# Kernel optimization log

Measured on AMD Instinct MI355X. Metric: run time of the kernel, lower is better.

The kernel has to match this reference:

```python
import jax, jax.numpy as jnp
import numpy as np

TEMP = 0.07
EPS = 1e-8
NUM_CLASSES = 7
THRESH = 0.3


def setup_inputs() -> dict:
    key = jax.random.key(0)
    k1, k2, k3, k4, k5 = jax.random.split(key, 5)
    N, H, E, C = 8192, 128, 256, NUM_CLASSES
    reps = jax.random.normal(k1, (N, H), dtype=jnp.float32)
    labels = jax.random.randint(k2, (N,), 0, C, dtype=jnp.int64 if jax.config.jax_enable_x64 else jnp.int32)
    centers = jax.random.normal(k3, (C, E), dtype=jnp.float32)
    fc_w = jax.random.normal(k4, (H, E), dtype=jnp.float32) * (1.0 / np.sqrt(E))
    fc_b = jax.random.normal(k5, (H,), dtype=jnp.float32) * 0.01
    return {"reps": reps, "labels": labels, "centers": centers, "fc_w": fc_w, "fc_b": fc_b}


def reference(reps, labels, centers, fc_w, fc_b):
    # fc(default_centers): [C, H]
    curr_centers = centers @ fc_w.T + fc_b
    pad_labels = jnp.arange(NUM_CLASSES, dtype=labels.dtype)

    all_reps = jnp.concatenate([reps, curr_centers], axis=0)      # [M, H]
    all_labels = jnp.concatenate([labels, pad_labels], axis=0)    # [M]
    B = reps.shape[0]
    M = all_reps.shape[0]

    # cosine similarity via normalized matmul (avoids [B,M,H] broadcast)
    norms = jnp.sqrt(jnp.sum(all_reps * all_reps, axis=-1))
    rn = all_reps / jnp.maximum(norms, 1e-8)[:, None]
    cos = rn[:B] @ rn.T                                           # [B, M]

    scores = (1.0 + cos) * 0.5 + EPS
    eye = (jnp.arange(B)[:, None] == jnp.arange(M)[None, :]).astype(scores.dtype)
    scores = scores * (1.0 - eye) / TEMP
    # torch uses .item() on the max -> a non-differentiable constant
    scores = scores - jax.lax.stop_gradient(jnp.max(scores))
    e = jnp.exp(scores)

    pos_mask = (labels[:, None] == all_labels[None, :]).astype(scores.dtype)  # [B, M]
    mask = 1.0 - eye

    pos_sum = jnp.sum(e * pos_mask * mask, axis=-1)
    neg_sum = jnp.sum(e * (1.0 - pos_mask), axis=-1)
    probs = pos_sum / (pos_sum + neg_sum)
    probs = probs / (jnp.sum(pos_mask * mask, axis=-1) + EPS)

    loss_vec = -jnp.log(probs + EPS)
    loss_mask = (loss_vec > THRESH).astype(loss_vec.dtype)
    denom = jax.lax.stop_gradient(jnp.sum(loss_mask)) + EPS
    loss = jnp.sum(loss_vec * loss_mask) / denom
    return loss
```

## Files before the change

kernel.cpp:

```cpp
#include <hip/hip_runtime.h>
#include <hip/hip_bf16.h>

#define BN 8192
#define MM 8199
#define MP 8208
#define HH 128
#define EE 256
#define NTILE 513
#define JCHUNKS 64
#define NUM_HIST 7

typedef __attribute__((ext_vector_type(8))) short short8;
typedef __attribute__((ext_vector_type(4))) float floatx4;

__global__ __launch_bounds__(256)
void centers_kernel(const float* __restrict__ centers,
                    const float* __restrict__ fc_w,
                    const float* __restrict__ fc_b,
                    float* __restrict__ curr) {
  int wid = threadIdx.x >> 6, lane = threadIdx.x & 63;
  int o = (blockIdx.x << 2) | wid;
  int c = o >> 7, h = o & 127;
  const float4* ce = (const float4*)(centers + c * EE);
  const float4* w  = (const float4*)(fc_w + h * EE);
  float4 a = ce[lane];
  float4 b = w[lane];
  float s = a.x * b.x + a.y * b.y + a.z * b.z + a.w * b.w;
#pragma unroll
  for (int m = 1; m < 64; m <<= 1) s += __shfl_xor(s, m);
  if (lane == 0) curr[o] = s + fc_b[h];
}

__global__ __launch_bounds__(256)
void norm_kernel(const float* __restrict__ reps,
                 const float* __restrict__ curr,
                 const int* __restrict__ labels,
                 __hip_bfloat16* __restrict__ rn,
                 int* __restrict__ labp) {
  int wid = threadIdx.x >> 6, lane = threadIdx.x & 63;
  int r = (blockIdx.x << 2) | wid;
  float2 v = make_float2(0.f, 0.f);
  if (r < BN)      v = ((const float2*)(reps + (size_t)r * HH))[lane];
  else if (r < MM) v = ((const float2*)(curr + (size_t)(r - BN) * HH))[lane];
  float ss = v.x * v.x + v.y * v.y;
#pragma unroll
  for (int m = 1; m < 64; m <<= 1) ss += __shfl_xor(ss, m);
  float inv = 1.0f / fmaxf(sqrtf(ss), 1e-8f);
  __hip_bfloat162 h2;
  h2.x = __float2bfloat16(v.x * inv);
  h2.y = __float2bfloat16(v.y * inv);
  ((__hip_bfloat162*)(rn + (size_t)r * HH))[lane] = h2;
  if (lane == 0) labp[r] = (r < BN) ? labels[r] : (r < MM ? r - BN : -1);
}

__global__ __launch_bounds__(256, 2)
void main_kernel(const __hip_bfloat16* __restrict__ rn,
                 const int* __restrict__ labp,
                 float* __restrict__ tot,
                 float* __restrict__ pos) {
  __shared__ float red[128];
  const int lane = threadIdx.x & 63;
  const int wid  = threadIdx.x >> 6;
  const int q = lane >> 4, col = lane & 15;
  const int ibase = blockIdx.x * 64;
  const int chunk = (blockIdx.y << 2) | wid;
  const short* rns = (const short*)rn;

  if (threadIdx.x < 128) red[threadIdx.x] = 0.f;

  short8 afrag[4][4];
#pragma unroll
  for (int it = 0; it < 4; ++it) {
    const short8* p = (const short8*)(rns + (size_t)(ibase + it * 16 + col) * HH + q * 8);
    afrag[it][0] = p[0];
    afrag[it][1] = p[4];
    afrag[it][2] = p[8];
    afrag[it][3] = p[12];
  }
  int labi[4][4];
#pragma unroll
  for (int it = 0; it < 4; ++it)
#pragma unroll
    for (int r = 0; r < 4; ++r)
      labi[it][r] = labp[ibase + it * 16 + q * 4 + r];

  float stot[4][4] = {};
  float spos[4][4] = {};
  const float K2 = 10.30496147f;

  const short* bptr = rns + (chunk * 16 + col) * HH + q * 8;
  const int* lptr = labp + chunk * 16 + col;

  for (int jb = chunk * 16; jb < MP; jb += 16 * JCHUNKS) {
    short8 b0 = ((const short8*)bptr)[0];
    short8 b1 = ((const short8*)bptr)[4];
    short8 b2 = ((const short8*)bptr)[8];
    short8 b3 = ((const short8*)bptr)[12];
    const int labj = *lptr;
    bptr += 16 * JCHUNKS * HH;
    lptr += 16 * JCHUNKS;
#pragma unroll
    for (int it = 0; it < 4; ++it) {
      floatx4 acc = {0.f, 0.f, 0.f, 0.f};
      acc = __builtin_amdgcn_mfma_f32_16x16x32_bf16(afrag[it][0], b0, acc, 0, 0, 0);
      acc = __builtin_amdgcn_mfma_f32_16x16x32_bf16(afrag[it][1], b1, acc, 0, 0, 0);
      acc = __builtin_amdgcn_mfma_f32_16x16x32_bf16(afrag[it][2], b2, acc, 0, 0, 0);
      acc = __builtin_amdgcn_mfma_f32_16x16x32_bf16(afrag[it][3], b3, acc, 0, 0, 0);
      const bool isdiag = (jb == ibase + it * 16);
#pragma unroll
      for (int r = 0; r < 4; ++r) {
        float e = exp2f(fmaf(acc[r], K2, -K2));
        if (isdiag && (col == q * 4 + r)) e = 0.f;
        stot[it][r] += e;
        spos[it][r] += (labj == labi[it][r]) ? e : 0.f;
      }
    }
  }

  __syncthreads();

#pragma unroll
  for (int it = 0; it < 4; ++it)
#pragma unroll
    for (int r = 0; r < 4; ++r) {
      float tt = stot[it][r], pp = spos[it][r];
#pragma unroll
      for (int m = 1; m <= 8; m <<= 1) {
        tt += __shfl_xor(tt, m);
        pp += __shfl_xor(pp, m);
      }
      if (col == 0) {
        int li = it * 16 + q * 4 + r;
        atomicAdd(&red[li], tt);
        atomicAdd(&red[64 + li], pp);
      }
    }
  __syncthreads();
  if (threadIdx.x < 64)       atomicAdd(&tot[ibase + threadIdx.x], red[threadIdx.x]);
  else if (threadIdx.x < 128) atomicAdd(&pos[ibase + threadIdx.x - 64], red[threadIdx.x]);
}

__global__ __launch_bounds__(1024)
void loss_kernel(const float* __restrict__ tot,
                 const float* __restrict__ pos,
                 const int* __restrict__ labels,
                 float* __restrict__ out) {
  __shared__ int hist[NUM_HIST];
  __shared__ float s1[16], s2[16];
  const int tid = threadIdx.x;
  const int lane = tid & 63, wid = tid >> 6;
  if (tid < NUM_HIST) hist[tid] = 0;
  __syncthreads();
  int cnt0 = 0, cnt1 = 0, cnt2 = 0, cnt3 = 0, cnt4 = 0, cnt5 = 0, cnt6 = 0;
  for (int i = tid; i < BN; i += 1024) {
    int lab = labels[i];
    unsigned long long m0 = __ballot(lab == 0);
    unsigned long long m1 = __ballot(lab == 1);
    unsigned long long m2 = __ballot(lab == 2);
    unsigned long long m3 = __ballot(lab == 3);
    unsigned long long m4 = __ballot(lab == 4);
    unsigned long long m5 = __ballot(lab == 5);
    unsigned long long m6 = __ballot(lab == 6);
    if (lane == 0) {
      cnt0 += __popcll(m0); cnt1 += __popcll(m1); cnt2 += __popcll(m2);
      cnt3 += __popcll(m3); cnt4 += __popcll(m4); cnt5 += __popcll(m5);
      cnt6 += __popcll(m6);
    }
  }
  if (lane == 0) {
    atomicAdd(&hist[0], cnt0); atomicAdd(&hist[1], cnt1);
    atomicAdd(&hist[2], cnt2); atomicAdd(&hist[3], cnt3);
    atomicAdd(&hist[4], cnt4); atomicAdd(&hist[5], cnt5);
    atomicAdd(&hist[6], cnt6);
  }
  __syncthreads();
  const float K2 = 10.30496147f;
  const float epad = exp2f(-K2);
  float lsum = 0.f, msum = 0.f;
  for (int i = tid; i < BN; i += 1024) {
    float t = tot[i] - 9.0f * epad;
    float p = pos[i];
    float c = (float)hist[labels[i]];
    float pr = (p / t) / (c + 1e-8f);
    float lv = -logf(pr + 1e-8f);
    if (lv > 0.3f) { lsum += lv; msum += 1.f; }
  }
#pragma unroll
  for (int m = 1; m < 64; m <<= 1) {
    lsum += __shfl_xor(lsum, m);
    msum += __shfl_xor(msum, m);
  }
  if (lane == 0) { s1[wid] = lsum; s2[wid] = msum; }
  __syncthreads();
  if (wid == 0) {
    float a = (lane < 16) ? s1[lane] : 0.f;
    float b = (lane < 16) ? s2[lane] : 0.f;
#pragma unroll
    for (int m = 1; m < 16; m <<= 1) {
      a += __shfl_xor(a, m);
      b += __shfl_xor(b, m);
    }
    if (lane == 0) out[0] = a / (b + 1e-8f);
  }
}

extern "C" void kernel_launch(void* const* d_in, const int* in_sizes, int n_in,
                              void* d_out, int out_size, void* d_ws, size_t ws_size,
                              hipStream_t stream) {
  const float* reps    = (const float*)d_in[0];
  const int*   labels  = (const int*)d_in[1];
  const float* centers = (const float*)d_in[2];
  const float* fc_w    = (const float*)d_in[3];
  const float* fc_b    = (const float*)d_in[4];
  float* out = (float*)d_out;

  char* ws = (char*)d_ws;
  float* curr = (float*)ws;
  int* labp   = (int*)(ws + 4096);
  __hip_bfloat16* rn = (__hip_bfloat16*)(ws + 40960);
  float* tot = (float*)(ws + 40960 + 2101248);
  float* pos = tot + BN;

  hipMemsetAsync(tot, 0, 2 * BN * sizeof(float), stream);
  centers_kernel<<<224, 256, 0, stream>>>(centers, fc_w, fc_b, curr);
  norm_kernel<<<2052, 256, 0, stream>>>(reps, curr, labels, rn, labp);
  main_kernel<<<dim3(128, 16), 256, 0, stream>>>(rn, labp, tot, pos);
  loss_kernel<<<1, 1024, 0, stream>>>(tot, pos, labels, out);
}
```

Baseline: 138.2 us.

## Fuse prep kernels and loss into main kernel, prefetch B fragments

Merges the centers projection and normalization into one prep kernel that also zeroes the accumulators, replacing the memset. The final loss reduction moves into the main kernel via a last-block-done atomic counter, which drops one launch. The main loop software-prefetches the next B fragment and uses the raw hardware exp2 intrinsic. These cut launch overhead and hide load latency, at the cost of relying on correct fence/atomic ordering in the last block.

```diff
diff --git a/kernel.cpp b/kernel.cpp
--- a/kernel.cpp
+++ b/kernel.cpp
@@ -6,59 +6,84 @@
 #define MP 8208
 #define HH 128
 #define EE 256
-#define NTILE 513
 #define JCHUNKS 64
+#define GX 128
+#define GY 16
+#define NBLK (GX * GY)
 #define NUM_HIST 7
 
 typedef __attribute__((ext_vector_type(8))) short short8;
 typedef __attribute__((ext_vector_type(4))) float floatx4;
 
 __global__ __launch_bounds__(256)
-void centers_kernel(const float* __restrict__ centers,
-                    const float* __restrict__ fc_w,
-                    const float* __restrict__ fc_b,
-                    float* __restrict__ curr) {
-  int wid = threadIdx.x >> 6, lane = threadIdx.x & 63;
-  int o = (blockIdx.x << 2) | wid;
-  int c = o >> 7, h = o & 127;
-  const float4* ce = (const float4*)(centers + c * EE);
-  const float4* w  = (const float4*)(fc_w + h * EE);
-  float4 a = ce[lane];
-  float4 b = w[lane];
-  float s = a.x * b.x + a.y * b.y + a.z * b.z + a.w * b.w;
-#pragma unroll
-  for (int m = 1; m < 64; m <<= 1) s += __shfl_xor(s, m);
-  if (lane == 0) curr[o] = s + fc_b[h];
-}
-
-__global__ __launch_bounds__(256)
-void norm_kernel(const float* __restrict__ reps,
-                 const float* __restrict__ curr,
+void prep_kernel(const float* __restrict__ reps,
                  const int* __restrict__ labels,
+                 const float* __restrict__ centers,
+                 const float* __restrict__ fc_w,
+                 const float* __restrict__ fc_b,
                  __hip_bfloat16* __restrict__ rn,
-                 int* __restrict__ labp) {
-  int wid = threadIdx.x >> 6, lane = threadIdx.x & 63;
-  int r = (blockIdx.x << 2) | wid;
-  float2 v = make_float2(0.f, 0.f);
-  if (r < BN)      v = ((const float2*)(reps + (size_t)r * HH))[lane];
-  else if (r < MM) v = ((const float2*)(curr + (size_t)(r - BN) * HH))[lane];
-  float ss = v.x * v.x + v.y * v.y;
-#pragma unroll
-  for (int m = 1; m < 64; m <<= 1) ss += __shfl_xor(ss, m);
-  float inv = 1.0f / fmaxf(sqrtf(ss), 1e-8f);
-  __hip_bfloat162 h2;
-  h2.x = __float2bfloat16(v.x * inv);
-  h2.y = __float2bfloat16(v.y * inv);
-  ((__hip_bfloat162*)(rn + (size_t)r * HH))[lane] = h2;
-  if (lane == 0) labp[r] = (r < BN) ? labels[r] : (r < MM ? r - BN : -1);
+                 int* __restrict__ labp,
+                 float* __restrict__ tot,
+                 int* __restrict__ bcount) {
+  const int wid = threadIdx.x >> 6, lane = threadIdx.x & 63;
+  const int b = blockIdx.x;
+  if (b < 2048) {
+    if (threadIdx.x < 8) tot[b * 8 + threadIdx.x] = 0.f;
+    const int r = b * 4 + wid;
+    float2 v = ((const float2*)(reps + (size_t)r * HH))[lane];
+    float ss = v.x * v.x + v.y * v.y;
+#pragma unroll
+    for (int m = 1; m < 64; m <<= 1) ss += __shfl_xor(ss, m);
+    float inv = 1.0f / fmaxf(sqrtf(ss), 1e-8f);
+    __hip_bfloat162 h2;
+    h2.x = __float2bfloat16(v.x * inv);
+    h2.y = __float2bfloat16(v.y * inv);
+    ((__hip_bfloat162*)(rn + (size_t)r * HH))[lane] = h2;
+    if (lane == 0) labp[r] = labels[r];
+  } else {
+    __shared__ float currs[7 * HH];
+    if (threadIdx.x == 0) *bcount = 0;
+    for (int o = threadIdx.x; o < 7 * HH; o += 256) {
+      int c = o >> 7, h = o & 127;
+      const float4* ce = (const float4*)(centers + c * EE);
+      const float4* w  = (const float4*)(fc_w + h * EE);
+      float s = 0.f;
+#pragma unroll 4
+      for (int j = 0; j < EE / 4; ++j) {
+        float4 a = ce[j], bb = w[j];
+        s += a.x * bb.x + a.y * bb.y + a.z * bb.z + a.w * bb.w;
+      }
+      currs[o] = s + fc_b[h];
+    }
+    __syncthreads();
+    for (int k = 0; k < 4; ++k) {
+      int c = wid * 4 + k;
+      int r = BN + c;
+      float2 v = make_float2(0.f, 0.f);
+      if (c < 7) v = ((const float2*)(currs + c * HH))[lane];
+      float ss = v.x * v.x + v.y * v.y;
+#pragma unroll
+      for (int m = 1; m < 64; m <<= 1) ss += __shfl_xor(ss, m);
+      float inv = 1.0f / fmaxf(sqrtf(ss), 1e-8f);
+      __hip_bfloat162 h2;
+      h2.x = __float2bfloat16(v.x * inv);
+      h2.y = __float2bfloat16(v.y * inv);
+      ((__hip_bfloat162*)(rn + (size_t)r * HH))[lane] = h2;
+      if (lane == 0) labp[r] = (r < MM) ? r - BN : -1;
+    }
+  }
 }
 
 __global__ __launch_bounds__(256, 2)
 void main_kernel(const __hip_bfloat16* __restrict__ rn,
                  const int* __restrict__ labp,
+                 const int* __restrict__ labels,
                  float* __restrict__ tot,
-                 float* __restrict__ pos) {
+                 float* __restrict__ pos,
+                 int* __restrict__ bcount,
+                 float* __restrict__ out) {
   __shared__ float red[128];
+  __shared__ int amlast;
   const int lane = threadIdx.x & 63;
   const int wid  = threadIdx.x >> 6;
   const int q = lane >> 4, col = lane & 15;
@@ -88,33 +113,45 @@
   float spos[4][4] = {};
   const float K2 = 10.30496147f;
 
-  const short* bptr = rns + (chunk * 16 + col) * HH + q * 8;
-  const int* lptr = labp + chunk * 16 + col;
-
-  for (int jb = chunk * 16; jb < MP; jb += 16 * JCHUNKS) {
-    short8 b0 = ((const short8*)bptr)[0];
-    short8 b1 = ((const short8*)bptr)[4];
-    short8 b2 = ((const short8*)bptr)[8];
-    short8 b3 = ((const short8*)bptr)[12];
-    const int labj = *lptr;
-    bptr += 16 * JCHUNKS * HH;
-    lptr += 16 * JCHUNKS;
+  const short* bptr = rns + (size_t)(chunk * 16 + col) * HH + q * 8;
+  short8 bc0 = ((const short8*)bptr)[0];
+  short8 bc1 = ((const short8*)bptr)[4];
+  short8 bc2 = ((const short8*)bptr)[8];
+  short8 bc3 = ((const short8*)bptr)[12];
+  int labj = labp[chunk * 16 + col];
+  int jb = chunk * 16;
+
+  while (true) {
+    const int jn = jb + 16 * JCHUNKS;
+    const bool more = (jn < MP);
+    const short* np = more ? (bptr + 16 * JCHUNKS * HH) : (rns + col * HH + q * 8);
+    short8 n0 = ((const short8*)np)[0];
+    short8 n1 = ((const short8*)np)[4];
+    short8 n2 = ((const short8*)np)[8];
+    short8 n3 = ((const short8*)np)[12];
+    const int labn = labp[more ? jn + col : col];
+
 #pragma unroll
     for (int it = 0; it < 4; ++it) {
       floatx4 acc = {0.f, 0.f, 0.f, 0.f};
-      acc = __builtin_amdgcn_mfma_f32_16x16x32_bf16(afrag[it][0], b0, acc, 0, 0, 0);
-      acc = __builtin_amdgcn_mfma_f32_16x16x32_bf16(afrag[it][1], b1, acc, 0, 0, 0);
-      acc = __builtin_amdgcn_mfma_f32_16x16x32_bf16(afrag[it][2], b2, acc, 0, 0, 0);
-      acc = __builtin_amdgcn_mfma_f32_16x16x32_bf16(afrag[it][3], b3, acc, 0, 0, 0);
+      acc = __builtin_amdgcn_mfma_f32_16x16x32_bf16(afrag[it][0], bc0, acc, 0, 0, 0);
+      acc = __builtin_amdgcn_mfma_f32_16x16x32_bf16(afrag[it][1], bc1, acc, 0, 0, 0);
+      acc = __builtin_amdgcn_mfma_f32_16x16x32_bf16(afrag[it][2], bc2, acc, 0, 0, 0);
+      acc = __builtin_amdgcn_mfma_f32_16x16x32_bf16(afrag[it][3], bc3, acc, 0, 0, 0);
       const bool isdiag = (jb == ibase + it * 16);
 #pragma unroll
       for (int r = 0; r < 4; ++r) {
-        float e = exp2f(fmaf(acc[r], K2, -K2));
+        float e = __builtin_amdgcn_exp2f(fmaf(acc[r], K2, -K2));
         if (isdiag && (col == q * 4 + r)) e = 0.f;
         stot[it][r] += e;
         spos[it][r] += (labj == labi[it][r]) ? e : 0.f;
       }
     }
+    if (!more) break;
+    jb = jn;
+    bptr = np;
+    bc0 = n0; bc1 = n1; bc2 = n2; bc3 = n3;
+    labj = labn;
   }
 
   __syncthreads();
@@ -138,21 +175,24 @@
   __syncthreads();
   if (threadIdx.x < 64)       atomicAdd(&tot[ibase + threadIdx.x], red[threadIdx.x]);
   else if (threadIdx.x < 128) atomicAdd(&pos[ibase + threadIdx.x - 64], red[threadIdx.x]);
-}
-
-__global__ __launch_bounds__(1024)
-void loss_kernel(const float* __restrict__ tot,
-                 const float* __restrict__ pos,
-                 const int* __restrict__ labels,
-                 float* __restrict__ out) {
+
+  __threadfence();
+  __syncthreads();
+  if (threadIdx.x == 0) {
+    int old = atomicAdd(bcount, 1);
+    amlast = (old == NBLK - 1) ? 1 : 0;
+  }
+  __syncthreads();
+  if (!amlast) return;
+  __threadfence();
+
   __shared__ int hist[NUM_HIST];
-  __shared__ float s1[16], s2[16];
+  __shared__ float s1[4], s2[4];
   const int tid = threadIdx.x;
-  const int lane = tid & 63, wid = tid >> 6;
   if (tid < NUM_HIST) hist[tid] = 0;
   __syncthreads();
-  int cnt0 = 0, cnt1 = 0, cnt2 = 0, cnt3 = 0, cnt4 = 0, cnt5 = 0, cnt6 = 0;
-  for (int i = tid; i < BN; i += 1024) {
+  int c0 = 0, c1 = 0, c2 = 0, c3 = 0, c4 = 0, c5 = 0, c6 = 0;
+  for (int i = tid; i < BN; i += 256) {
     int lab = labels[i];
     unsigned long long m0 = __ballot(lab == 0);
     unsigned long long m1 = __ballot(lab == 1);
@@ -162,24 +202,22 @@
     unsigned long long m5 = __ballot(lab == 5);
     unsigned long long m6 = __ballot(lab == 6);
     if (lane == 0) {
-      cnt0 += __popcll(m0); cnt1 += __popcll(m1); cnt2 += __popcll(m2);
-      cnt3 += __popcll(m3); cnt4 += __popcll(m4); cnt5 += __popcll(m5);
-      cnt6 += __popcll(m6);
+      c0 += __popcll(m0); c1 += __popcll(m1); c2 += __popcll(m2);
+      c3 += __popcll(m3); c4 += __popcll(m4); c5 += __popcll(m5);
+      c6 += __popcll(m6);
     }
   }
   if (lane == 0) {
-    atomicAdd(&hist[0], cnt0); atomicAdd(&hist[1], cnt1);
-    atomicAdd(&hist[2], cnt2); atomicAdd(&hist[3], cnt3);
-    atomicAdd(&hist[4], cnt4); atomicAdd(&hist[5], cnt5);
-    atomicAdd(&hist[6], cnt6);
-  }
-  __syncthreads();
-  const float K2 = 10.30496147f;
-  const float epad = exp2f(-K2);
+    atomicAdd(&hist[0], c0); atomicAdd(&hist[1], c1); atomicAdd(&hist[2], c2);
+    atomicAdd(&hist[3], c3); atomicAdd(&hist[4], c4); atomicAdd(&hist[5], c5);
+    atomicAdd(&hist[6], c6);
+  }
+  __syncthreads();
+  const float epad9 = 9.0f * __builtin_amdgcn_exp2f(-K2);
   float lsum = 0.f, msum = 0.f;
-  for (int i = tid; i < BN; i += 1024) {
-    float t = tot[i] - 9.0f * epad;
-    float p = pos[i];
+  for (int i = tid; i < BN; i += 256) {
+    float t = __hip_atomic_load(&tot[i], __ATOMIC_RELAXED, __HIP_MEMORY_SCOPE_AGENT) - epad9;
+    float p = __hip_atomic_load(&pos[i], __ATOMIC_RELAXED, __HIP_MEMORY_SCOPE_AGENT);
     float c = (float)hist[labels[i]];
     float pr = (p / t) / (c + 1e-8f);
     float lv = -logf(pr + 1e-8f);
@@ -192,15 +230,10 @@
   }
   if (lane == 0) { s1[wid] = lsum; s2[wid] = msum; }
   __syncthreads();
-  if (wid == 0) {
-    float a = (lane < 16) ? s1[lane] : 0.f;
-    float b = (lane < 16) ? s2[lane] : 0.f;
-#pragma unroll
-    for (int m = 1; m < 16; m <<= 1) {
-      a += __shfl_xor(a, m);
-      b += __shfl_xor(b, m);
-    }
-    if (lane == 0) out[0] = a / (b + 1e-8f);
+  if (tid == 0) {
+    float a = s1[0] + s1[1] + s1[2] + s1[3];
+    float b = s2[0] + s2[1] + s2[2] + s2[3];
+    out[0] = a / (b + 1e-8f);
   }
 }
 
@@ -215,15 +248,13 @@
   float* out = (float*)d_out;
 
   char* ws = (char*)d_ws;
-  float* curr = (float*)ws;
+  int* bcount = (int*)(ws + 3584);
   int* labp   = (int*)(ws + 4096);
   __hip_bfloat16* rn = (__hip_bfloat16*)(ws + 40960);
   float* tot = (float*)(ws + 40960 + 2101248);
   float* pos = tot + BN;
 
-  hipMemsetAsync(tot, 0, 2 * BN * sizeof(float), stream);
-  centers_kernel<<<224, 256, 0, stream>>>(centers, fc_w, fc_b, curr);
-  norm_kernel<<<2052, 256, 0, stream>>>(reps, curr, labels, rn, labp);
-  main_kernel<<<dim3(128, 16), 256, 0, stream>>>(rn, labp, tot, pos);
-  loss_kernel<<<1, 1024, 0, stream>>>(tot, pos, labels, out);
+  prep_kernel<<<2049, 256, 0, stream>>>(reps, labels, centers, fc_w, fc_b,
+                                        rn, labp, tot, bcount);
+  main_kernel<<<dim3(GX, GY), 256, 0, stream>>>(rn, labp, labels, tot, pos, bcount, out);
 }
```

Measured after the change: 280.9 us. 2.03x slower.

## Fuse memset, center projection and normalization into one prep kernel; halve main tile rows

Applied to the files above, without the earlier changes.

Merges the memset, the centers projection kernel and the norm kernel into a single prep kernel. The last block computes the 7 projected centers in shared memory and normalizes them, which removes two launches and a memset. The main kernel now handles 32 rows per block instead of 64, doubling the grid to 256x16 for more parallelism. The price is more redundant B-fragment loads across blocks and a serial single-block centers computation.

```diff
diff --git a/kernel.cpp b/kernel.cpp
--- a/kernel.cpp
+++ b/kernel.cpp
@@ -6,51 +6,69 @@
 #define MP 8208
 #define HH 128
 #define EE 256
-#define NTILE 513
 #define JCHUNKS 64
+#define GX 256
+#define GY 16
 #define NUM_HIST 7
 
 typedef __attribute__((ext_vector_type(8))) short short8;
 typedef __attribute__((ext_vector_type(4))) float floatx4;
 
 __global__ __launch_bounds__(256)
-void centers_kernel(const float* __restrict__ centers,
-                    const float* __restrict__ fc_w,
-                    const float* __restrict__ fc_b,
-                    float* __restrict__ curr) {
-  int wid = threadIdx.x >> 6, lane = threadIdx.x & 63;
-  int o = (blockIdx.x << 2) | wid;
-  int c = o >> 7, h = o & 127;
-  const float4* ce = (const float4*)(centers + c * EE);
-  const float4* w  = (const float4*)(fc_w + h * EE);
-  float4 a = ce[lane];
-  float4 b = w[lane];
-  float s = a.x * b.x + a.y * b.y + a.z * b.z + a.w * b.w;
-#pragma unroll
-  for (int m = 1; m < 64; m <<= 1) s += __shfl_xor(s, m);
-  if (lane == 0) curr[o] = s + fc_b[h];
-}
-
-__global__ __launch_bounds__(256)
-void norm_kernel(const float* __restrict__ reps,
-                 const float* __restrict__ curr,
+void prep_kernel(const float* __restrict__ reps,
                  const int* __restrict__ labels,
+                 const float* __restrict__ centers,
+                 const float* __restrict__ fc_w,
+                 const float* __restrict__ fc_b,
                  __hip_bfloat16* __restrict__ rn,
-                 int* __restrict__ labp) {
-  int wid = threadIdx.x >> 6, lane = threadIdx.x & 63;
-  int r = (blockIdx.x << 2) | wid;
-  float2 v = make_float2(0.f, 0.f);
-  if (r < BN)      v = ((const float2*)(reps + (size_t)r * HH))[lane];
-  else if (r < MM) v = ((const float2*)(curr + (size_t)(r - BN) * HH))[lane];
-  float ss = v.x * v.x + v.y * v.y;
-#pragma unroll
-  for (int m = 1; m < 64; m <<= 1) ss += __shfl_xor(ss, m);
-  float inv = 1.0f / fmaxf(sqrtf(ss), 1e-8f);
-  __hip_bfloat162 h2;
-  h2.x = __float2bfloat16(v.x * inv);
-  h2.y = __float2bfloat16(v.y * inv);
-  ((__hip_bfloat162*)(rn + (size_t)r * HH))[lane] = h2;
-  if (lane == 0) labp[r] = (r < BN) ? labels[r] : (r < MM ? r - BN : -1);
+                 int* __restrict__ labp,
+                 float* __restrict__ tot) {
+  const int wid = threadIdx.x >> 6, lane = threadIdx.x & 63;
+  const int b = blockIdx.x;
+  if (b < 2048) {
+    if (threadIdx.x < 8) tot[b * 8 + threadIdx.x] = 0.f;
+    const int r = b * 4 + wid;
+    float2 v = ((const float2*)(reps + (size_t)r * HH))[lane];
+    float ss = v.x * v.x + v.y * v.y;
+#pragma unroll
+    for (int m = 1; m < 64; m <<= 1) ss += __shfl_xor(ss, m);
+    float inv = 1.0f / fmaxf(sqrtf(ss), 1e-8f);
+    __hip_bfloat162 h2;
+    h2.x = __float2bfloat16(v.x * inv);
+    h2.y = __float2bfloat16(v.y * inv);
+    ((__hip_bfloat162*)(rn + (size_t)r * HH))[lane] = h2;
+    if (lane == 0) labp[r] = labels[r];
+  } else {
+    __shared__ float currs[7 * HH];
+    for (int o = threadIdx.x; o < 7 * HH; o += 256) {
+      int c = o >> 7, h = o & 127;
+      const float4* ce = (const float4*)(centers + c * EE);
+      const float4* w  = (const float4*)(fc_w + h * EE);
+      float s = 0.f;
+#pragma unroll 4
+      for (int j = 0; j < EE / 4; ++j) {
+        float4 a = ce[j], bb = w[j];
+        s += a.x * bb.x + a.y * bb.y + a.z * bb.z + a.w * bb.w;
+      }
+      currs[o] = s + fc_b[h];
+    }
+    __syncthreads();
+    for (int k = 0; k < 4; ++k) {
+      int c = wid * 4 + k;
+      int r = BN + c;
+      float2 v = make_float2(0.f, 0.f);
+      if (c < 7) v = ((const float2*)(currs + c * HH))[lane];
+      float ss = v.x * v.x + v.y * v.y;
+#pragma unroll
+      for (int m = 1; m < 64; m <<= 1) ss += __shfl_xor(ss, m);
+      float inv = 1.0f / fmaxf(sqrtf(ss), 1e-8f);
+      __hip_bfloat162 h2;
+      h2.x = __float2bfloat16(v.x * inv);
+      h2.y = __float2bfloat16(v.y * inv);
+      ((__hip_bfloat162*)(rn + (size_t)r * HH))[lane] = h2;
+      if (lane == 0) labp[r] = (r < MM) ? r - BN : -1;
+    }
+  }
 }
 
 __global__ __launch_bounds__(256, 2)
@@ -58,37 +76,37 @@
                  const int* __restrict__ labp,
                  float* __restrict__ tot,
                  float* __restrict__ pos) {
-  __shared__ float red[128];
+  __shared__ float red[64];
   const int lane = threadIdx.x & 63;
   const int wid  = threadIdx.x >> 6;
   const int q = lane >> 4, col = lane & 15;
-  const int ibase = blockIdx.x * 64;
+  const int ibase = blockIdx.x * 32;
   const int chunk = (blockIdx.y << 2) | wid;
   const short* rns = (const short*)rn;
 
-  if (threadIdx.x < 128) red[threadIdx.x] = 0.f;
-
-  short8 afrag[4][4];
-#pragma unroll
-  for (int it = 0; it < 4; ++it) {
+  if (threadIdx.x < 64) red[threadIdx.x] = 0.f;
+
+  short8 afrag[2][4];
+#pragma unroll
+  for (int it = 0; it < 2; ++it) {
     const short8* p = (const short8*)(rns + (size_t)(ibase + it * 16 + col) * HH + q * 8);
     afrag[it][0] = p[0];
     afrag[it][1] = p[4];
     afrag[it][2] = p[8];
     afrag[it][3] = p[12];
   }
-  int labi[4][4];
-#pragma unroll
-  for (int it = 0; it < 4; ++it)
+  int labi[2][4];
+#pragma unroll
+  for (int it = 0; it < 2; ++it)
 #pragma unroll
     for (int r = 0; r < 4; ++r)
       labi[it][r] = labp[ibase + it * 16 + q * 4 + r];
 
-  float stot[4][4] = {};
-  float spos[4][4] = {};
+  float stot[2][4] = {};
+  float spos[2][4] = {};
   const float K2 = 10.30496147f;
 
-  const short* bptr = rns + (chunk * 16 + col) * HH + q * 8;
+  const short* bptr = rns + (size_t)(chunk * 16 + col) * HH + q * 8;
   const int* lptr = labp + chunk * 16 + col;
 
   for (int jb = chunk * 16; jb < MP; jb += 16 * JCHUNKS) {
@@ -100,7 +118,7 @@
     bptr += 16 * JCHUNKS * HH;
     lptr += 16 * JCHUNKS;
 #pragma unroll
-    for (int it = 0; it < 4; ++it) {
+    for (int it = 0; it < 2; ++it) {
       floatx4 acc = {0.f, 0.f, 0.f, 0.f};
       acc = __builtin_amdgcn_mfma_f32_16x16x32_bf16(afrag[it][0], b0, acc, 0, 0, 0);
       acc = __builtin_amdgcn_mfma_f32_16x16x32_bf16(afrag[it][1], b1, acc, 0, 0, 0);
@@ -120,7 +138,7 @@
   __syncthreads();
 
 #pragma unroll
-  for (int it = 0; it < 4; ++it)
+  for (int it = 0; it < 2; ++it)
 #pragma unroll
     for (int r = 0; r < 4; ++r) {
       float tt = stot[it][r], pp = spos[it][r];
@@ -132,12 +150,12 @@
       if (col == 0) {
         int li = it * 16 + q * 4 + r;
         atomicAdd(&red[li], tt);
-        atomicAdd(&red[64 + li], pp);
-      }
-    }
-  __syncthreads();
-  if (threadIdx.x < 64)       atomicAdd(&tot[ibase + threadIdx.x], red[threadIdx.x]);
-  else if (threadIdx.x < 128) atomicAdd(&pos[ibase + threadIdx.x - 64], red[threadIdx.x]);
+        atomicAdd(&red[32 + li], pp);
+      }
+    }
+  __syncthreads();
+  if (threadIdx.x < 32)      atomicAdd(&tot[ibase + threadIdx.x], red[threadIdx.x]);
+  else if (threadIdx.x < 64) atomicAdd(&pos[ibase + threadIdx.x - 32], red[threadIdx.x]);
 }
 
 __global__ __launch_bounds__(1024)
@@ -151,7 +169,7 @@
   const int lane = tid & 63, wid = tid >> 6;
   if (tid < NUM_HIST) hist[tid] = 0;
   __syncthreads();
-  int cnt0 = 0, cnt1 = 0, cnt2 = 0, cnt3 = 0, cnt4 = 0, cnt5 = 0, cnt6 = 0;
+  int c0 = 0, c1 = 0, c2 = 0, c3 = 0, c4 = 0, c5 = 0, c6 = 0;
   for (int i = tid; i < BN; i += 1024) {
     int lab = labels[i];
     unsigned long long m0 = __ballot(lab == 0);
@@ -162,23 +180,22 @@
     unsigned long long m5 = __ballot(lab == 5);
     unsigned long long m6 = __ballot(lab == 6);
     if (lane == 0) {
-      cnt0 += __popcll(m0); cnt1 += __popcll(m1); cnt2 += __popcll(m2);
-      cnt3 += __popcll(m3); cnt4 += __popcll(m4); cnt5 += __popcll(m5);
-      cnt6 += __popcll(m6);
+      c0 += __popcll(m0); c1 += __popcll(m1); c2 += __popcll(m2);
+      c3 += __popcll(m3); c4 += __popcll(m4); c5 += __popcll(m5);
+      c6 += __popcll(m6);
     }
   }
   if (lane == 0) {
-    atomicAdd(&hist[0], cnt0); atomicAdd(&hist[1], cnt1);
-    atomicAdd(&hist[2], cnt2); atomicAdd(&hist[3], cnt3);
-    atomicAdd(&hist[4], cnt4); atomicAdd(&hist[5], cnt5);
-    atomicAdd(&hist[6], cnt6);
+    atomicAdd(&hist[0], c0); atomicAdd(&hist[1], c1); atomicAdd(&hist[2], c2);
+    atomicAdd(&hist[3], c3); atomicAdd(&hist[4], c4); atomicAdd(&hist[5], c5);
+    atomicAdd(&hist[6], c6);
   }
   __syncthreads();
   const float K2 = 10.30496147f;
-  const float epad = exp2f(-K2);
+  const float epad9 = 9.0f * exp2f(-K2);
   float lsum = 0.f, msum = 0.f;
   for (int i = tid; i < BN; i += 1024) {
-    float t = tot[i] - 9.0f * epad;
+    float t = tot[i] - epad9;
     float p = pos[i];
     float c = (float)hist[labels[i]];
     float pr = (p / t) / (c + 1e-8f);
@@ -215,15 +232,12 @@
   float* out = (float*)d_out;
 
   char* ws = (char*)d_ws;
-  float* curr = (float*)ws;
   int* labp   = (int*)(ws + 4096);
   __hip_bfloat16* rn = (__hip_bfloat16*)(ws + 40960);
   float* tot = (float*)(ws + 40960 + 2101248);
   float* pos = tot + BN;
 
-  hipMemsetAsync(tot, 0, 2 * BN * sizeof(float), stream);
-  centers_kernel<<<224, 256, 0, stream>>>(centers, fc_w, fc_b, curr);
-  norm_kernel<<<2052, 256, 0, stream>>>(reps, curr, labels, rn, labp);
-  main_kernel<<<dim3(128, 16), 256, 0, stream>>>(rn, labp, tot, pos);
+  prep_kernel<<<2049, 256, 0, stream>>>(reps, labels, centers, fc_w, fc_b, rn, labp, tot);
+  main_kernel<<<dim3(GX, GY), 256, 0, stream>>>(rn, labp, tot, pos);
   loss_kernel<<<1, 1024, 0, stream>>>(tot, pos, labels, out);
 }
```

New measurement: 185.7 us. 34.4% more time.
